# Kernel optimization log

Measured on AMD Instinct MI355X. Metric: run time of the kernel, lower is better.

Reference implementation:

```python
import jax, jax.numpy as jnp
import numpy as np

WEIGHT = 1e-7
SIGMA_RGB = 15.0
SCALE = 0.5


def _nearest_resize(x, oh, ow):
    # PyTorch F.interpolate mode='nearest': src_idx = floor(dst * in/out)
    n, c, h, w = x.shape
    yi = (jnp.arange(oh) * (h / oh)).astype(jnp.int32)
    xi = (jnp.arange(ow) * (w / ow)).astype(jnp.int32)
    return x[:, :, yi][:, :, :, xi]


def _bilinear_resize(x, oh, ow):
    # PyTorch bilinear, align_corners=False: src = max((i+0.5)*in/out - 0.5, 0)
    n, k, h, w = x.shape

    def idx(o, s):
        src = jnp.maximum((jnp.arange(o, dtype=jnp.float32) + 0.5) * (s / o) - 0.5, 0.0)
        lo = jnp.floor(src).astype(jnp.int32)
        hi = jnp.minimum(lo + 1, s - 1)
        return lo, hi, src - lo

    ylo, yhi, fy = idx(oh, h)
    xlo, xhi, fx = idx(ow, w)
    top = x[:, :, ylo][:, :, :, xlo] * (1.0 - fx) + x[:, :, ylo][:, :, :, xhi] * fx
    bot = x[:, :, yhi][:, :, :, xlo] * (1.0 - fx) + x[:, :, yhi][:, :, :, xhi] * fx
    return top * (1.0 - fy)[:, None] + bot * fy[:, None]


def _bilateral_AS(feat, seg):
    # feat: [P,3] color features / sigma_rgb; seg: [K,P]
    # exact Gaussian color bilateral filter (what the permutohedral lattice approximates)
    sq = jnp.sum(feat * feat, axis=-1)                      # [P]
    d2 = sq[:, None] + sq[None, :] - 2.0 * (feat @ feat.T)  # [P,P]
    Kmat = jnp.exp(-0.5 * jnp.maximum(d2, 0.0))             # [P,P], symmetric
    return seg @ Kmat                                        # [K,P]


def setup_inputs() -> dict:
    key = jax.random.key(0)
    k1, k2 = jax.random.split(key)
    images = jax.random.uniform(k1, (4, 3, 128, 128), dtype=jnp.float32) * 255.0
    logits = jax.random.normal(k2, (4, 21, 128, 128), dtype=jnp.float32)
    segmentations = jax.nn.softmax(logits, axis=1)
    return {"images": images, "segmentations": segmentations}


def reference(images, segmentations):
    n, c, h, w = images.shape
    oh, ow = int(h * SCALE), int(w * SCALE)
    simg = _nearest_resize(images, oh, ow)            # [N,3,oh,ow]
    sseg = _bilinear_resize(segmentations, oh, ow)    # [N,K,oh,ow]
    P = oh * ow
    feats = simg.reshape(n, c, P).transpose(0, 2, 1) / SIGMA_RGB  # [N,P,3]
    segs = sseg.reshape(n, sseg.shape[1], P)                      # [N,K,P]
    AS = jax.vmap(_bilateral_AS)(feats, segs)                     # [N,K,P]
    loss = -jnp.sum(segs * AS) / jnp.float32(n)
    return (WEIGHT * loss).reshape(1)
```

## Files before the change

### kernel.cpp

```cpp
#include <hip/hip_runtime.h>


#define N_BATCH 4
#define IH 128
#define IW 128
#define P 4096
#define KC 21

using short8   = __attribute__((ext_vector_type(8))) short;
using floatx16 = __attribute__((ext_vector_type(16))) float;

static constexpr float INV_SIGMA = 1.0f / 15.0f;
static constexpr float LOG2E     = 1.4426950408889634f;
static constexpr float OUT_SCALE = -1e-7f / 4.0f;

#define ARGA_OFF  0
#define ARGB_OFF  (N_BATCH * P * 32)
#define SEGLO_OFF (2 * N_BATCH * P * 32)
#define SEGHI_OFF (3 * N_BATCH * P * 32)

#define NFEAT (N_BATCH * P)
#define NSEG2 (N_BATCH * KC * P / 2)

__device__ __forceinline__ ushort f2bf(float x) {
    unsigned u = __builtin_bit_cast(unsigned, x);
    unsigned r = (u + 0x7FFFu + ((u >> 16) & 1u)) >> 16;
    return (ushort)r;
}
__device__ __forceinline__ float bf2f(ushort h) {
    return __builtin_bit_cast(float, (unsigned)h << 16);
}

__device__ __forceinline__ void gload16(const void* g, void* l) {
    __builtin_amdgcn_global_load_lds(
        (const __attribute__((address_space(1))) unsigned int*)g,
        (__attribute__((address_space(3))) unsigned int*)l, 16, 0, 0);
}

__global__ void crf_prep(const float* __restrict__ img,
                         const float* __restrict__ seg,
                         char* __restrict__ wsb,
                         float* __restrict__ out)
{
    int t = blockIdx.x * blockDim.x + threadIdx.x;
    if (t < NFEAT) {
        if (t == 0) out[0] = 0.0f;

        int n = t >> 12;
        int p = t & (P - 1);
        int y = p >> 6, x = p & 63;

        const float* ib = img + (size_t)n * 3 * IH * IW + (size_t)(2 * y) * IW + 2 * x;
        float f0 = ib[0] * INV_SIGMA;
        float f1 = ib[IH * IW] * INV_SIGMA;
        float f2 = ib[2 * IH * IW] * INV_SIGMA;
        float h = 0.5f * (f0 * f0 + f1 * f1 + f2 * f2);

        float fa0 = f0 * LOG2E, fa1 = f1 * LOG2E, fa2 = f2 * LOG2E;
        ushort ah0 = f2bf(fa0), ah1 = f2bf(fa1), ah2 = f2bf(fa2);
        ushort al0 = f2bf(fa0 - bf2f(ah0));
        ushort al1 = f2bf(fa1 - bf2f(ah1));
        ushort al2 = f2bf(fa2 - bf2f(ah2));
        float nhL = -h * LOG2E;
        ushort nhh = f2bf(nhL), nhl = f2bf(nhL - bf2f(nhh));
        ushort bh0 = f2bf(f0), bh1 = f2bf(f1), bh2 = f2bf(f2);
        ushort bl0 = f2bf(f0 - bf2f(bh0));
        ushort bl1 = f2bf(f1 - bf2f(bh1));
        ushort bl2 = f2bf(f2 - bf2f(bh2));
        float hL = h * LOG2E;
        ushort hbh = f2bf(hL), hbl = f2bf(hL - bf2f(hbh));

        const ushort ONE = 0x3F80, NEG1 = 0xBF80;
        ushort rA[16] = {ah0, ah1, ah2, ah0, ah1, ah2, al0, al1, al2, al0, al1, al2,
                         nhh, nhl, NEG1, NEG1};
        ushort rB[16] = {bh0, bh1, bh2, bl0, bl1, bl2, bh0, bh1, bh2, bl0, bl1, bl2,
                         ONE, ONE, hbh, hbl};

        short8 vA0, vA1, vB0, vB1;
#pragma unroll
        for (int j = 0; j < 8; ++j) {
            vA0[j] = (short)rA[j];     vA1[j] = (short)rA[8 + j];
            vB0[j] = (short)rB[j];     vB1[j] = (short)rB[8 + j];
        }
        short8* dA = (short8*)(wsb + ARGA_OFF + (size_t)t * 32);
        dA[0] = vA0; dA[1] = vA1;
        short8* dB = (short8*)(wsb + ARGB_OFF + (size_t)t * 32);
        dB[0] = vB0; dB[1] = vB1;

        char* hp = wsb + SEGHI_OFF + (size_t)t * 32;
        *(ushort*)(hp + 10) = 0;
        *(uint*)(hp + 12) = 0;
        *(size_t*)(hp + 16) = 0;
        *(size_t*)(hp + 24) = 0;
    } else if (t < NFEAT + NSEG2) {
        int u = t - NFEAT;
        int pp = (u & 2047) * 2;
        int nk = u >> 11;
        int n = nk / 21;
        int k = nk - n * 21;
        int y = pp >> 6, x0 = pp & 63;

        const float* r0 = seg + (size_t)nk * IH * IW + (size_t)(2 * y) * IW + 2 * x0;
        float4 a = *(const float4*)r0;
        float4 b = *(const float4*)(r0 + IW);
        float v0 = 0.25f * ((a.x + a.y) + (b.x + b.y));
        float v1 = 0.25f * ((a.z + a.w) + (b.z + b.w));
        size_t off = (k < 16) ? (SEGLO_OFF + (size_t)(n * P + pp) * 32 + k * 2)
                              : (SEGHI_OFF + (size_t)(n * P + pp) * 32 + (k - 16) * 2);
        char* d = wsb + off;
        *(ushort*)d = f2bf(v0);
        *(ushort*)(d + 32) = f2bf(v1);
    }
}

__device__ __forceinline__ void tilestep(short8 aA, short8 aL, short8 aH,
                                         short8 bA, short8 bL, short8 bH,
                                         float& acc)
{
    floatx16 z = {0.0f};
    floatx16 g  = __builtin_amdgcn_mfma_f32_32x32x16_bf16(aL, bL, z, 0, 0, 0);
    g           = __builtin_amdgcn_mfma_f32_32x32x16_bf16(aH, bH, g, 0, 0, 0);
    floatx16 ar = __builtin_amdgcn_mfma_f32_32x32x16_bf16(aA, bA, z, 0, 0, 0);
    float s = 0.0f;
#pragma unroll
    for (int r = 0; r < 16; ++r)
        s += __builtin_amdgcn_exp2f(ar[r]) * g[r];
    acc += s;
}

__global__ __launch_bounds__(256, 4) void crf_pair(const char* __restrict__ wsb,
                                                   float* __restrict__ out)
{
    int n = blockIdx.z;
    int bp = blockIdx.y;
    int bx = blockIdx.x;
    int wave = threadIdx.x >> 6;
    int lane = threadIdx.x & 63;
    int m31 = lane & 31;
    int hi  = lane >> 5;

    const char* argA = wsb + ARGA_OFF  + (size_t)n * P * 32;
    const char* argB = wsb + ARGB_OFF  + (size_t)n * P * 32;
    const char* segL = wsb + SEGLO_OFF + (size_t)n * P * 32;
    const char* segH = wsb + SEGHI_OFF + (size_t)n * P * 32;

    int cnt0 = 128 - 4 * bp;
    int i0t = 4 * bp + wave;
    int i1t = 124 - 4 * bp + wave;
    int rd = m31 * 32 + hi * 16;

    short8 aA0 = *(const short8*)(argA + (size_t)i0t * 1024 + rd);
    short8 aL0 = *(const short8*)(segL + (size_t)i0t * 1024 + rd);
    short8 aH0 = *(const short8*)(segH + (size_t)i0t * 1024 + rd);
    short8 aA1 = *(const short8*)(argA + (size_t)i1t * 1024 + rd);
    short8 aL1 = *(const short8*)(segL + (size_t)i1t * 1024 + rd);
    short8 aH1 = *(const short8*)(segH + (size_t)i1t * 1024 + rd);

    __shared__ __align__(16) char lbuf[2 * 3072];
    __shared__ float wsum[4];

    int nst = (bx < 4) ? 9 : 8;

    {
        int m = bx;
        int j = (m < cnt0) ? (4 * bp + m) : (m - 4);
        if (wave == 0)      gload16(argB + (size_t)j * 1024 + lane * 16, lbuf);
        else if (wave == 1) gload16(segL + (size_t)j * 1024 + lane * 16, lbuf + 1024);
        else if (wave == 2) gload16(segH + (size_t)j * 1024 + lane * 16, lbuf + 2048);
    }
    __syncthreads();

    float acc1 = 0.0f, acc2 = 0.0f;
    for (int t = 0; t < nst; ++t) {
        int cur = (t & 1) * 3072;
        if (t + 1 < nst) {
            int mn = bx + 16 * (t + 1);
            int jn = (mn < cnt0) ? (4 * bp + mn) : (mn - 4);
            int nxt = 3072 - cur;
            if (wave == 0)      gload16(argB + (size_t)jn * 1024 + lane * 16, lbuf + nxt);
            else if (wave == 1) gload16(segL + (size_t)jn * 1024 + lane * 16, lbuf + nxt + 1024);
            else if (wave == 2) gload16(segH + (size_t)jn * 1024 + lane * 16, lbuf + nxt + 2048);
        }

        int m = bx + 16 * t;
        int j = (m < cnt0) ? (4 * bp + m) : (m - 4);
        short8 bA = *(const short8*)(lbuf + cur + rd);
        short8 bL = *(const short8*)(lbuf + cur + 1024 + rd);
        short8 bH = *(const short8*)(lbuf + cur + 2048 + rd);

        if (m < cnt0) {
            if (i0t < j)       tilestep(aA0, aL0, aH0, bA, bL, bH, acc2);
            else if (i0t == j) tilestep(aA0, aL0, aH0, bA, bL, bH, acc1);
        } else {
            if (i1t < j)       tilestep(aA1, aL1, aH1, bA, bL, bH, acc2);
            else if (i1t == j) tilestep(aA1, aL1, aH1, bA, bL, bH, acc1);
        }
        __syncthreads();
    }

    float part = 2.0f * acc2 + acc1;
#pragma unroll
    for (int off = 32; off > 0; off >>= 1)
        part += __shfl_down(part, off, 64);
    if (lane == 0) wsum[wave] = part;
    __syncthreads();
    if (threadIdx.x == 0)
        atomicAdd(out, ((wsum[0] + wsum[1]) + (wsum[2] + wsum[3])) * OUT_SCALE);
}

extern "C" void kernel_launch(void* const* d_in, const int* in_sizes, int n_in,
                              void* d_out, int out_size, void* d_ws, size_t ws_size,
                              hipStream_t stream)
{
    const float* images = (const float*)d_in[0];
    const float* segm   = (const float*)d_in[1];
    float* out = (float*)d_out;
    char* wsb = (char*)d_ws;

    int prep_threads = NFEAT + NSEG2;
    crf_prep<<<dim3((prep_threads + 255) / 256), dim3(256), 0, stream>>>(
        images, segm, wsb, out);
    crf_pair<<<dim3(16, 16, N_BATCH), dim3(256), 0, stream>>>(wsb, out);
}
```

Measured before the change: 79.89 us.

## Fuse prep and pair kernels via cooperative launch with grid sync

Merges the preprocessing and pairwise kernels into one cooperative kernel of 1024 blocks that runs the prep phase, does a grid-wide sync, then runs the pairwise phase. The goal is to remove the second kernel launch and the gap between the two kernels. Prep needs 16384+172032 threads, which is 736 blocks, so 1024 blocks cover it. If the cooperative launch fails, it falls back to the original two launches. The risk is grid-sync overhead and the cooperative-launch residency limits, since 1024 blocks at 4 per CU need 256 CUs.

```diff
diff --git a/kernel.cpp b/kernel.cpp
--- a/kernel.cpp
+++ b/kernel.cpp
@@ -1,5 +1,8 @@
 #include <hip/hip_runtime.h>
-
+#include <hip/hip_cooperative_groups.h>
+
+
+namespace cg = cooperative_groups;
 
 #define N_BATCH 4
 #define IH 128
@@ -37,12 +40,12 @@
         (__attribute__((address_space(3))) unsigned int*)l, 16, 0, 0);
 }
 
-__global__ void crf_prep(const float* __restrict__ img,
-                         const float* __restrict__ seg,
-                         char* __restrict__ wsb,
-                         float* __restrict__ out)
-{
-    int t = blockIdx.x * blockDim.x + threadIdx.x;
+__device__ __forceinline__ void phaseA(int t,
+                                       const float* __restrict__ img,
+                                       const float* __restrict__ seg,
+                                       char* __restrict__ wsb,
+                                       float* __restrict__ out)
+{
     if (t < NFEAT) {
         if (t == 0) out[0] = 0.0f;
 
@@ -128,12 +131,10 @@
     acc += s;
 }
 
-__global__ __launch_bounds__(256, 4) void crf_pair(const char* __restrict__ wsb,
-                                                   float* __restrict__ out)
-{
-    int n = blockIdx.z;
-    int bp = blockIdx.y;
-    int bx = blockIdx.x;
+__device__ __forceinline__ void phaseB(int n, int bp, int bx,
+                                       const char* __restrict__ wsb,
+                                       float* __restrict__ out)
+{
     int wave = threadIdx.x >> 6;
     int lane = threadIdx.x & 63;
     int m31 = lane & 31;
@@ -171,10 +172,10 @@
     __syncthreads();
 
     float acc1 = 0.0f, acc2 = 0.0f;
-    for (int t = 0; t < nst; ++t) {
-        int cur = (t & 1) * 3072;
-        if (t + 1 < nst) {
-            int mn = bx + 16 * (t + 1);
+    for (int st = 0; st < nst; ++st) {
+        int cur = (st & 1) * 3072;
+        if (st + 1 < nst) {
+            int mn = bx + 16 * (st + 1);
             int jn = (mn < cnt0) ? (4 * bp + mn) : (mn - 4);
             int nxt = 3072 - cur;
             if (wave == 0)      gload16(argB + (size_t)jn * 1024 + lane * 16, lbuf + nxt);
@@ -182,7 +183,7 @@
             else if (wave == 2) gload16(segH + (size_t)jn * 1024 + lane * 16, lbuf + nxt + 2048);
         }
 
-        int m = bx + 16 * t;
+        int m = bx + 16 * st;
         int j = (m < cnt0) ? (4 * bp + m) : (m - 4);
         short8 bA = *(const short8*)(lbuf + cur + rd);
         short8 bL = *(const short8*)(lbuf + cur + 1024 + rd);
@@ -208,6 +209,31 @@
         atomicAdd(out, ((wsum[0] + wsum[1]) + (wsum[2] + wsum[3])) * OUT_SCALE);
 }
 
+__global__ __launch_bounds__(256, 4) void crf_fused(const float* __restrict__ img,
+                                                    const float* __restrict__ seg,
+                                                    char* __restrict__ wsb,
+                                                    float* __restrict__ out)
+{
+    int bid = blockIdx.x;
+    phaseA(bid * 256 + (int)threadIdx.x, img, seg, wsb, out);
+    cg::this_grid().sync();
+    phaseB(bid >> 8, (bid >> 4) & 15, bid & 15, wsb, out);
+}
+
+__global__ __launch_bounds__(256) void crf_prep_k(const float* __restrict__ img,
+                                                  const float* __restrict__ seg,
+                                                  char* __restrict__ wsb,
+                                                  float* __restrict__ out)
+{
+    phaseA(blockIdx.x * 256 + (int)threadIdx.x, img, seg, wsb, out);
+}
+
+__global__ __launch_bounds__(256, 4) void crf_pair_k(const char* __restrict__ wsb,
+                                                     float* __restrict__ out)
+{
+    phaseB(blockIdx.z, blockIdx.y, blockIdx.x, wsb, out);
+}
+
 extern "C" void kernel_launch(void* const* d_in, const int* in_sizes, int n_in,
                               void* d_out, int out_size, void* d_ws, size_t ws_size,
                               hipStream_t stream)
@@ -217,8 +243,13 @@
     float* out = (float*)d_out;
     char* wsb = (char*)d_ws;
 
-    int prep_threads = NFEAT + NSEG2;
-    crf_prep<<<dim3((prep_threads + 255) / 256), dim3(256), 0, stream>>>(
-        images, segm, wsb, out);
-    crf_pair<<<dim3(16, 16, N_BATCH), dim3(256), 0, stream>>>(wsb, out);
-}
+    void* kargs[4] = {(void*)&images, (void*)&segm, (void*)&wsb, (void*)&out};
+    hipError_t err = hipLaunchCooperativeKernel((void*)crf_fused, dim3(1024),
+                                                dim3(256), kargs, 0, stream);
+    if (err != hipSuccess) {
+        int prep_threads = NFEAT + NSEG2;
+        crf_prep_k<<<dim3((prep_threads + 255) / 256), dim3(256), 0, stream>>>(
+            images, segm, wsb, out);
+        crf_pair_k<<<dim3(16, 16, N_BATCH), dim3(256), 0, stream>>>(wsb, out);
+    }
+}
```

New measurement: 188.9 us. 136% more time.
